# Kernel optimization log

Measured on AMD Instinct MI355X. Metric: run time of the kernel, lower is better.

## Reference

```python
import jax, jax.numpy as jnp
import numpy as np

D_MODEL = 128
NUM_HEADS = 8
DEPTH = D_MODEL // NUM_HEADS
NEG = -1e9


def _dense_params(key, d_in, d_out):
    kw, kb = jax.random.split(key)
    # Glorot-uniform like keras Dense default
    lim = np.sqrt(6.0 / (d_in + d_out))
    w = jax.random.uniform(kw, (d_in, d_out), jnp.float32, -lim, lim)
    b = jnp.zeros((d_out,), jnp.float32)
    return w, b


def setup_inputs() -> dict:
    key = jax.random.key(0)
    ks = jax.random.split(key, 16)
    B, N, M, d = 256, 128, 128, D_MODEL
    inp = {
        'x_self': jax.random.normal(ks[0], (B, N, d), jnp.float32),
        'adj_self': jax.random.randint(ks[1], (B, N, N), 0, 2, jnp.int32),
        'mask_self': jnp.ones((B, N), jnp.int32),
        'x_cross': jax.random.normal(ks[2], (B, M, d), jnp.float32),
        'mask_cross': jnp.ones((B, M), jnp.int32),
    }
    names = ['wq_s', 'wk_s', 'wv_s', 'wo_s', 'wq_c', 'wk_c', 'wv_c', 'wo_c']
    for i, nm in enumerate(names):
        w, b = _dense_params(ks[3 + i], d, d)
        inp[nm] = w
        inp['b' + nm[1:]] = b
    wg, bg = _dense_params(ks[12], 3 * d, d)
    inp['wg'] = wg
    inp['bg'] = bg
    return inp


def _split_heads(x):
    B, N, _ = x.shape
    return x.reshape(B, N, NUM_HEADS, DEPTH).transpose(0, 2, 1, 3)  # [B,H,N,depth]


def _merge_heads(x):
    B, H, N, Dp = x.shape
    return x.transpose(0, 2, 1, 3).reshape(B, N, H * Dp)


def _attention(q, k, v, mask, adj=None):
    # q,k,v: [B,H,Nq,depth]; mask: [B,Nk]; adj: [B,Nq,Nk] or None
    logits = jnp.einsum('bhqd,bhkd->bhqk', q, k) / jnp.sqrt(jnp.float32(DEPTH))
    if adj is not None:
        logits = logits + ((1.0 - adj.astype(jnp.float32)) * NEG)[:, None, :, :]
    logits = logits + ((1.0 - mask.astype(jnp.float32)) * NEG)[:, None, None, :]
    w = jax.nn.softmax(logits, axis=-1)
    return jnp.einsum('bhqk,bhkd->bhqd', w, v)


def reference(x_self, adj_self, mask_self, x_cross, mask_cross,
              wq_s, bq_s, wk_s, bk_s, wv_s, bv_s, wo_s, bo_s,
              wq_c, bq_c, wk_c, bk_c, wv_c, bv_c, wo_c, bo_c,
              wg, bg):
    # Self attention (adjacency + padding mask)
    q_s = _split_heads(x_self @ wq_s + bq_s)
    k_s = _split_heads(x_self @ wk_s + bk_s)
    v_s = _split_heads(x_self @ wv_s + bv_s)
    out_s = _merge_heads(_attention(q_s, k_s, v_s, mask_self, adj_self)) @ wo_s + bo_s
    # Cross attention (padding mask only); dropout inactive at inference
    q_c = _split_heads(x_self @ wq_c + bq_c)
    k_c = _split_heads(x_cross @ wk_c + bk_c)
    v_c = _split_heads(x_cross @ wv_c + bv_c)
    out_c = _merge_heads(_attention(q_c, k_c, v_c, mask_cross)) @ wo_c + bo_c
    # Sigmoid gate fusion
    gate = jax.nn.sigmoid(jnp.concatenate([x_self, out_s, out_c], axis=-1) @ wg + bg)
    return (1.0 - gate) * out_s + gate * out_c
```

## Files before the change

kernel.cpp:

```cpp
#include <hip/hip_runtime.h>
#include <hip/hip_bf16.h>

typedef _Float16 f16_t;
typedef __attribute__((ext_vector_type(8))) _Float16 f16x8;
typedef __attribute__((ext_vector_type(4))) float f32x4;
typedef __attribute__((ext_vector_type(16))) float f32x16;

__device__ __forceinline__ f16x8 cvt8(const float* p) {
  float4 v0 = *(const float4*)p;
  float4 v1 = *(const float4*)(p + 4);
  f16x8 a;
  a[0] = (f16_t)v0.x; a[1] = (f16_t)v0.y; a[2] = (f16_t)v0.z; a[3] = (f16_t)v0.w;
  a[4] = (f16_t)v1.x; a[5] = (f16_t)v1.y; a[6] = (f16_t)v1.z; a[7] = (f16_t)v1.w;
  return a;
}

__global__ __launch_bounds__(256) void prep_kernel(
    const float* wq_s, const float* wk_s, const float* wv_s,
    const float* wq_c, const float* wk_c, const float* wv_c,
    const float* wo_s, const float* wo_c, const float* wg,
    const float* bos, const float* boc, const float* bgin,
    f16_t* WT, float* bgp)
{
  const int b = blockIdx.x;
  const int tid = threadIdx.x;
  if (b < 11) {
    __shared__ float t[128][129];
    const float* src; f16_t* dst; int ostride;
    switch (b) {
      case 0: src = wq_s; break; case 1: src = wk_s; break;
      case 2: src = wv_s; break; case 3: src = wq_c; break;
      case 4: src = wk_c; break; case 5: src = wv_c; break;
      case 6: src = wo_s; break; case 7: src = wo_c; break;
      default: src = wg + (size_t)(b - 8) * 16384; break;
    }
    if (b < 8) { dst = WT + (size_t)b * 16384; ostride = 128; }
    else       { dst = WT + 8 * 16384 + (b - 8) * 128; ostride = 384; }
#pragma unroll
    for (int i = 0; i < 64; ++i) {
      const int idx = tid + i * 256;
      t[idx & 127][idx >> 7] = src[idx];
    }
    __syncthreads();
#pragma unroll
    for (int i = 0; i < 64; ++i) {
      const int idx = tid + i * 256;
      const int c = idx >> 7, r = idx & 127;
      dst[(size_t)c * ostride + r] = (f16_t)t[c][r];
    }
  } else if (b < 13) {
    const int matsel = b - 11;
    const float* wo = matsel ? wo_c : wo_s;
    const int joff = 128 + matsel * 128;
    f16_t* dst = WT + (size_t)(11 + matsel) * 16384;
    const int wv = tid >> 6, ln = tid & 63, l15 = ln & 15, g = ln >> 4;
    f32x4 acc[2][8];
#pragma unroll
    for (int mm = 0; mm < 2; ++mm)
#pragma unroll
      for (int nt = 0; nt < 8; ++nt) acc[mm][nt] = (f32x4){0.f, 0.f, 0.f, 0.f};
#pragma unroll
    for (int kt = 0; kt < 4; ++kt) {
      f16x8 a[2];
#pragma unroll
      for (int mm = 0; mm < 2; ++mm) {
        const int crow = wv * 32 + mm * 16 + l15;
#pragma unroll
        for (int jj = 0; jj < 8; ++jj)
          a[mm][jj] = (f16_t)wg[(size_t)(joff + kt * 32 + g * 8 + jj) * 128 + crow];
      }
#pragma unroll
      for (int nt = 0; nt < 8; ++nt) {
        f16x8 bf = cvt8(wo + (size_t)(nt * 16 + l15) * 128 + kt * 32 + g * 8);
        acc[0][nt] = __builtin_amdgcn_mfma_f32_16x16x32_f16(a[0], bf, acc[0][nt], 0, 0, 0);
        acc[1][nt] = __builtin_amdgcn_mfma_f32_16x16x32_f16(a[1], bf, acc[1][nt], 0, 0, 0);
      }
    }
#pragma unroll
    for (int mm = 0; mm < 2; ++mm)
#pragma unroll
      for (int nt = 0; nt < 8; ++nt)
#pragma unroll
        for (int r = 0; r < 4; ++r) {
          const int c = wv * 32 + mm * 16 + g * 4 + r;
          dst[(size_t)c * 128 + nt * 16 + l15] = (f16_t)acc[mm][nt][r];
        }
  } else {
    if (tid < 128) {
      float acc = bgin[tid];
      for (int j = 0; j < 128; ++j)
        acc += bos[j] * wg[(size_t)(128 + j) * 128 + tid] +
               boc[j] * wg[(size_t)(256 + j) * 128 + tid];
      bgp[tid] = acc;
    }
  }
}

template <int NW>
__device__ __forceinline__ void proj_body(
    const float* __restrict__ A, const f16_t* __restrict__ WT, int blk, int tid,
    const float* b0, f16_t* Y0, const float* b1, f16_t* Y1,
    const float* b2, f16_t* Y2, const float* b3, f16_t* Y3)
{
  const int wv = tid >> 6, ln = tid & 63, l15 = ln & 15, g = ln >> 4;
  const int rowgrp = wv & 1, colgrp = wv >> 1;
  const size_t arow = (size_t)blk * 32 + rowgrp * 16 + l15;

  f32x4 acc[NW][4];
#pragma unroll
  for (int i = 0; i < NW; ++i)
#pragma unroll
    for (int nt = 0; nt < 4; ++nt) acc[i][nt] = (f32x4){0.f, 0.f, 0.f, 0.f};

#pragma unroll
  for (int kt = 0; kt < 4; ++kt) {
    f16x8 a = cvt8(A + arow * 128 + kt * 32 + g * 8);
#pragma unroll
    for (int i = 0; i < NW; ++i)
#pragma unroll
      for (int nt = 0; nt < 4; ++nt) {
        f16x8 bfr = *(const f16x8*)(WT + (size_t)i * 16384 +
                     (size_t)(colgrp * 64 + nt * 16 + l15) * 128 + kt * 32 + g * 8);
        acc[i][nt] = __builtin_amdgcn_mfma_f32_16x16x32_f16(a, bfr, acc[i][nt], 0, 0, 0);
      }
  }

  const size_t orow0 = (size_t)blk * 32 + rowgrp * 16 + g * 4;
#pragma unroll
  for (int i = 0; i < NW; ++i) {
    const float* bp = (i == 0) ? b0 : (i == 1) ? b1 : (i == 2) ? b2 : b3;
    f16_t* Y = (i == 0) ? Y0 : (i == 1) ? Y1 : (i == 2) ? Y2 : Y3;
#pragma unroll
    for (int nt = 0; nt < 4; ++nt) {
      const int col = colgrp * 64 + nt * 16 + l15;
      const float bv = bp[col];
#pragma unroll
      for (int r = 0; r < 4; ++r)
        Y[(orow0 + r) * 128 + col] = (f16_t)(acc[i][nt][r] + bv);
    }
  }
}

__global__ __launch_bounds__(256) void projall_kernel(
    const float* __restrict__ Xs, const float* __restrict__ Xc,
    const f16_t* __restrict__ WT,
    const float* bq_s, const float* bk_s, const float* bv_s, const float* bq_c,
    const float* bk_c, const float* bv_c,
    f16_t* qs, f16_t* ks, f16_t* vs, f16_t* qc, f16_t* kc, f16_t* vc)
{
  if (blockIdx.x < 1024)
    proj_body<4>(Xs, WT, blockIdx.x, threadIdx.x,
                 bq_s, qs, bk_s, ks, bv_s, vs, bq_c, qc);
  else
    proj_body<2>(Xc, WT + 4 * 16384, blockIdx.x - 1024, threadIdx.x,
                 bk_c, kc, bv_c, vc, nullptr, nullptr, nullptr, nullptr);
}

__global__ __launch_bounds__(256) void attn4_kernel(
    const f16_t* __restrict__ Qs, const f16_t* __restrict__ Ks,
    const f16_t* __restrict__ Vs, f16_t* __restrict__ Os,
    const f16_t* __restrict__ Qc, const f16_t* __restrict__ Kc,
    const f16_t* __restrict__ Vc, f16_t* __restrict__ Oc,
    const int* __restrict__ adj, const int* __restrict__ mask_s,
    const int* __restrict__ mask_c)
{
  __shared__ __align__(16) f16_t Qh[128 * 24];
  __shared__ __align__(16) f16_t Kh[128 * 24];
  __shared__ __align__(16) f16_t Vt[16 * 136];
  __shared__ __align__(16) f16_t Pl[128 * 128];
  __shared__ float larr[128];
  __shared__ unsigned mw[4];
  __shared__ unsigned adjw[128 * 4];

  const bool self = blockIdx.x < 2048;
  const int bid = blockIdx.x & 2047;
  const int h = bid >> 8;
  const int bb = bid & 255;
  const int tid = threadIdx.x;
  const size_t base = (size_t)bb * 16384 + h * 16;
  const f16_t* Q = self ? Qs : Qc;
  const f16_t* K = self ? Ks : Kc;
  const f16_t* V = self ? Vs : Vc;
  f16_t* O = self ? Os : Oc;
  const int* mask = self ? mask_s : mask_c;

  {
    const int r = tid >> 1, hf = tid & 1;
    f16x8 qv = *(const f16x8*)(Q + base + (size_t)r * 128 + hf * 8);
    *(f16x8*)&Qh[r * 24 + hf * 8] = qv;
    f16x8 kv = *(const f16x8*)(K + base + (size_t)r * 128 + hf * 8);
    *(f16x8*)&Kh[r * 24 + hf * 8] = kv;
    f16x8 vv = *(const f16x8*)(V + base + (size_t)r * 128 + hf * 8);
#pragma unroll
    for (int j = 0; j < 8; ++j) Vt[(hf * 8 + j) * 136 + r] = vv[j];
  }
  if (tid < 128) {
    unsigned long long bm = __ballot(mask[bb * 128 + tid] != 0);
    if ((tid & 63) == 0) {
      mw[(tid >> 6) * 2 + 0] = (unsigned)bm;
      mw[(tid >> 6) * 2 + 1] = (unsigned)(bm >> 32);
    }
  }
  if (self) {
    const int r = tid >> 1, hf = tid & 1;
    const int4* ap = (const int4*)(adj + ((size_t)bb * 128 + r) * 128 + hf * 64);
    unsigned w0 = 0, w1 = 0;
#pragma unroll
    for (int i = 0; i < 8; ++i) {
      int4 a = ap[i];
      unsigned m4 = (a.x != 0 ? 1u : 0u) | (a.y != 0 ? 2u : 0u) |
                    (a.z != 0 ? 4u : 0u) | (a.w != 0 ? 8u : 0u);
      w0 |= m4 << (i * 4);
    }
#pragma unroll
    for (int i = 8; i < 16; ++i) {
      int4 a = ap[i];
      unsigned m4 = (a.x != 0 ? 1u : 0u) | (a.y != 0 ? 2u : 0u) |
                    (a.z != 0 ? 4u : 0u) | (a.w != 0 ? 8u : 0u);
      w1 |= m4 << ((i - 8) * 4);
    }
    adjw[r * 4 + hf * 2 + 0] = w0;
    adjw[r * 4 + hf * 2 + 1] = w1;
  }
  __syncthreads();

  const int ln = tid & 63;
  const int wv = tid >> 6;
  const int l31 = ln & 31;
  const int hh = ln >> 5;
  const int q = wv * 32 + l31;

  f32x16 zero16;
#pragma unroll
  for (int j = 0; j < 16; ++j) zero16[j] = 0.f;
  const f16x8 bq = *(const f16x8*)&Qh[q * 24 + hh * 8];
  f32x16 st[4];
#pragma unroll
  for (int kt = 0; kt < 4; ++kt) {
    const f16x8 ak = *(const f16x8*)&Kh[(kt * 32 + l31) * 24 + hh * 8];
    st[kt] = __builtin_amdgcn_mfma_f32_32x32x16_f16(ak, bq, zero16, 0, 0, 0);
  }

  unsigned aw[4];
#pragma unroll
  for (int kt = 0; kt < 4; ++kt)
    aw[kt] = self ? (adjw[q * 4 + kt] & mw[kt]) : mw[kt];

  const int swz = (q & 7) << 4;
  float l = 0.f;
#pragma unroll
  for (int kt = 0; kt < 4; ++kt) {
#pragma unroll
    for (int r2 = 0; r2 < 8; ++r2) {
      const int r = r2 * 2;
      const int koff = (r & 3) + 8 * (r >> 2) + 4 * hh;
      float e0 = __expf(st[kt][r]     * 0.25f - 8.f);
      float e1 = __expf(st[kt][r + 1] * 0.25f - 8.f);
      float p0 = ((aw[kt] >> koff) & 1u) ? e0 : 0.f;
      float p1 = ((aw[kt] >> (koff + 1)) & 1u) ? e1 : 0.f;
      l += p0 + p1;
      unsigned short u0 = __builtin_bit_cast(unsigned short, (f16_t)p0);
      unsigned short u1 = __builtin_bit_cast(unsigned short, (f16_t)p1);
      unsigned pk = (unsigned)u0 | ((unsigned)u1 << 16);
      const int key = kt * 32 + koff;
      *(unsigned*)((char*)Pl + q * 256 + ((key * 2) ^ swz)) = pk;
    }
  }
  l += __shfl_xor(l, 32);
  if (hh == 0) larr[q] = l;
  __syncthreads();

  const int l15 = ln & 15;
  const int g4 = ln >> 4;
  const int qa0 = wv * 32 + l15;
  const int qa1 = qa0 + 16;
  const int swz0 = (qa0 & 7) << 4;
  const int swz1 = (qa1 & 7) << 4;
  f32x4 o0 = (f32x4){0.f, 0.f, 0.f, 0.f};
  f32x4 o1 = (f32x4){0.f, 0.f, 0.f, 0.f};
#pragma unroll
  for (int kt = 0; kt < 4; ++kt) {
    const f16x8 bv = *(const f16x8*)&Vt[l15 * 136 + kt * 32 + g4 * 8];
    const f16x8 p0 = *(const f16x8*)((char*)Pl + qa0 * 256 + ((kt * 64 + g4 * 16) ^ swz0));
    const f16x8 p1 = *(const f16x8*)((char*)Pl + qa1 * 256 + ((kt * 64 + g4 * 16) ^ swz1));
    o0 = __builtin_amdgcn_mfma_f32_16x16x32_f16(p0, bv, o0, 0, 0, 0);
    o1 = __builtin_amdgcn_mfma_f32_16x16x32_f16(p1, bv, o1, 0, 0, 0);
  }
#pragma unroll
  for (int rr = 0; rr < 4; ++rr) {
    const int q0 = wv * 32 + g4 * 4 + rr;
    const int q1 = q0 + 16;
    O[base + (size_t)q0 * 128 + l15] = (f16_t)(o0[rr] / larr[q0]);
    O[base + (size_t)q1 * 128 + l15] = (f16_t)(o1[rr] / larr[q1]);
  }
}

__global__ __launch_bounds__(256) void outgate2_kernel(
    const f16_t* __restrict__ AS, const f16_t* __restrict__ AC,
    const float* __restrict__ X, const f16_t* __restrict__ WT,
    const float* __restrict__ bos, const float* __restrict__ boc,
    const float* __restrict__ bgp, float* __restrict__ OUT)
{
  const int tid = threadIdx.x;
  const int wv = tid >> 6, ln = tid & 63, l15 = ln & 15, g = ln >> 4;
  const int rowgrp = wv & 1, colgrp = wv >> 1;
  const size_t arow = (size_t)blockIdx.x * 32 + rowgrp * 16 + l15;
  const f16_t* WoS = WT + 6 * 16384;
  const f16_t* WoC = WT + 7 * 16384;
  const f16_t* WgT = WT + 8 * 16384;
  const f16_t* W2T = WT + 11 * 16384;
  const f16_t* W3T = WT + 12 * 16384;

  f32x4 accS[4], accC[4], accG[4];
#pragma unroll
  for (int nt = 0; nt < 4; ++nt) {
    accS[nt] = (f32x4){0.f, 0.f, 0.f, 0.f};
    accC[nt] = (f32x4){0.f, 0.f, 0.f, 0.f};
    accG[nt] = (f32x4){0.f, 0.f, 0.f, 0.f};
  }

#pragma unroll
  for (int kt = 0; kt < 4; ++kt) {
    const size_t ko = kt * 32 + g * 8;
    f16x8 aS = *(const f16x8*)(AS + arow * 128 + ko);
    f16x8 aC = *(const f16x8*)(AC + arow * 128 + ko);
    f16x8 aX = cvt8(X + arow * 128 + ko);
#pragma unroll
    for (int nt = 0; nt < 4; ++nt) {
      const size_t col = colgrp * 64 + nt * 16 + l15;
      f16x8 bS = *(const f16x8*)(WoS + col * 128 + ko);
      f16x8 bC = *(const f16x8*)(WoC + col * 128 + ko);
      f16x8 b2 = *(const f16x8*)(W2T + col * 128 + ko);
      f16x8 b3 = *(const f16x8*)(W3T + col * 128 + ko);
      f16x8 bX = *(const f16x8*)(WgT + col * 384 + ko);
      accS[nt] = __builtin_amdgcn_mfma_f32_16x16x32_f16(aS, bS, accS[nt], 0, 0, 0);
      accC[nt] = __builtin_amdgcn_mfma_f32_16x16x32_f16(aC, bC, accC[nt], 0, 0, 0);
      accG[nt] = __builtin_amdgcn_mfma_f32_16x16x32_f16(aX, bX, accG[nt], 0, 0, 0);
      accG[nt] = __builtin_amdgcn_mfma_f32_16x16x32_f16(aS, b2, accG[nt], 0, 0, 0);
      accG[nt] = __builtin_amdgcn_mfma_f32_16x16x32_f16(aC, b3, accG[nt], 0, 0, 0);
    }
  }

  const size_t orow0 = (size_t)blockIdx.x * 32 + rowgrp * 16 + g * 4;
#pragma unroll
  for (int nt = 0; nt < 4; ++nt) {
    const int col = colgrp * 64 + nt * 16 + l15;
    const float bS = bos[col], bC = boc[col], bG = bgp[col];
#pragma unroll
    for (int r = 0; r < 4; ++r) {
      const float os = accS[nt][r] + bS;
      const float oc = accC[nt][r] + bC;
      const float gv = 1.f / (1.f + __expf(-(accG[nt][r] + bG)));
      OUT[(orow0 + r) * 128 + col] = (1.f - gv) * os + gv * oc;
    }
  }
}

extern "C" void kernel_launch(void* const* d_in, const int* in_sizes, int n_in,
                              void* d_out, int out_size, void* d_ws, size_t ws_size,
                              hipStream_t stream)
{
  const float* x_self  = (const float*)d_in[0];
  const int*   adj     = (const int*)d_in[1];
  const int*   mask_s  = (const int*)d_in[2];
  const float* x_cross = (const float*)d_in[3];
  const int*   mask_c  = (const int*)d_in[4];
  const float* wq_s = (const float*)d_in[5];
  const float* bq_s = (const float*)d_in[6];
  const float* wk_s = (const float*)d_in[7];
  const float* bk_s = (const float*)d_in[8];
  const float* wv_s = (const float*)d_in[9];
  const float* bv_s = (const float*)d_in[10];
  const float* wo_s = (const float*)d_in[11];
  const float* bo_s = (const float*)d_in[12];
  const float* wq_c = (const float*)d_in[13];
  const float* bq_c = (const float*)d_in[14];
  const float* wk_c = (const float*)d_in[15];
  const float* bk_c = (const float*)d_in[16];
  const float* wv_c = (const float*)d_in[17];
  const float* bv_c = (const float*)d_in[18];
  const float* wo_c = (const float*)d_in[19];
  const float* bo_c = (const float*)d_in[20];
  const float* wg   = (const float*)d_in[21];
  const float* bg   = (const float*)d_in[22];
  float* out = (float*)d_out;

  const size_t SZ = (size_t)256 * 128 * 128;
  f16_t* w16 = (f16_t*)d_ws;
  f16_t* qs  = w16 + 0 * SZ;
  f16_t* ks  = w16 + 1 * SZ;
  f16_t* vs  = w16 + 2 * SZ;
  f16_t* qc  = w16 + 3 * SZ;
  f16_t* kc  = w16 + 4 * SZ;
  f16_t* vc  = w16 + 5 * SZ;
  f16_t* as_ = w16 + 6 * SZ;
  f16_t* ac_ = w16 + 7 * SZ;
  f16_t* WT  = w16 + 8 * SZ;
  float* bgp = (float*)(WT + 13 * 16384);

  prep_kernel<<<14, 256, 0, stream>>>(wq_s, wk_s, wv_s, wq_c, wk_c, wv_c,
                                      wo_s, wo_c, wg, bo_s, bo_c, bg, WT, bgp);
  projall_kernel<<<2048, 256, 0, stream>>>(x_self, x_cross, WT,
                                           bq_s, bk_s, bv_s, bq_c, bk_c, bv_c,
                                           qs, ks, vs, qc, kc, vc);
  attn4_kernel<<<4096, 256, 0, stream>>>(qs, ks, vs, as_, qc, kc, vc, ac_,
                                         adj, mask_s, mask_c);
  outgate2_kernel<<<1024, 256, 0, stream>>>(as_, ac_, x_self, WT,
                                            bo_s, bo_c, bgp, out);
}
```

Baseline: 159.2 us.

## Fuse projections, both attentions and output gate into one per-batch kernel

Replaces the projection, attention and output-gate kernels with a single kernel: one 512-thread block per batch element. Q/K/V and the attention outputs now live in swizzled LDS buffers instead of f16 global intermediates, and each wave walks all 8 heads for its 16 query rows. This is meant to remove the global write and re-read of eight intermediate tensors and two kernel launches. The cost is about 144KB of LDS per block, so likely one block per CU and only 256 blocks, plus a long serial chain of GEMM and attention phases separated by barriers. Weights are still read from global/L2 inside every block.

```diff
diff --git a/kernel.cpp b/kernel.cpp
--- a/kernel.cpp
+++ b/kernel.cpp
@@ -4,7 +4,6 @@
 typedef _Float16 f16_t;
 typedef __attribute__((ext_vector_type(8))) _Float16 f16x8;
 typedef __attribute__((ext_vector_type(4))) float f32x4;
-typedef __attribute__((ext_vector_type(16))) float f32x16;
 
 __device__ __forceinline__ f16x8 cvt8(const float* p) {
   float4 v0 = *(const float4*)p;
@@ -96,262 +95,250 @@
   }
 }
 
-template <int NW>
-__device__ __forceinline__ void proj_body(
-    const float* __restrict__ A, const f16_t* __restrict__ WT, int blk, int tid,
-    const float* b0, f16_t* Y0, const float* b1, f16_t* Y1,
-    const float* b2, f16_t* Y2, const float* b3, f16_t* Y3)
-{
+template <bool TRANSP>
+__device__ __forceinline__ void gemm_w(
+    const f16x8 afr[4], const f16_t* __restrict__ W, const float* __restrict__ bias,
+    char* Ob, int l15, int g, int wv)
+{
+  f32x4 acc[8];
+#pragma unroll
+  for (int nt = 0; nt < 8; ++nt) acc[nt] = (f32x4){0.f, 0.f, 0.f, 0.f};
+#pragma unroll
+  for (int nt = 0; nt < 8; ++nt)
+#pragma unroll
+    for (int kt = 0; kt < 4; ++kt) {
+      f16x8 b = *(const f16x8*)(W + (size_t)(nt * 16 + l15) * 128 + kt * 32 + g * 8);
+      acc[nt] = __builtin_amdgcn_mfma_f32_16x16x32_f16(afr[kt], b, acc[nt], 0, 0, 0);
+    }
+#pragma unroll
+  for (int nt = 0; nt < 8; ++nt) {
+    const int col = nt * 16 + l15;
+    const float bv = bias[col];
+#pragma unroll
+    for (int r = 0; r < 4; ++r) {
+      const int row = wv * 16 + g * 4 + r;
+      const f16_t v = (f16_t)(acc[nt][r] + bv);
+      if (TRANSP)
+        *(f16_t*)(Ob + col * 256 + ((row * 2) ^ ((col & 7) << 4))) = v;
+      else
+        *(f16_t*)(Ob + row * 256 + ((col * 2) ^ ((row & 7) << 4))) = v;
+    }
+  }
+}
+
+__device__ __forceinline__ void attn_wave(
+    char* Qb, const char* Kb, const char* Vtb, const unsigned aw[4],
+    char* Pw, int l15, int g, int wv)
+{
+  const int q = wv * 16 + l15;
+  const int qsw = (q & 7) << 4;
+  const int psw = (l15 & 7) << 4;
+  const f32x4 zero = (f32x4){0.f, 0.f, 0.f, 0.f};
+
+#pragma unroll
+  for (int h = 0; h < 8; ++h) {
+    f16x8 bq = {0, 0, 0, 0, 0, 0, 0, 0};
+    if (g < 2) bq = *(const f16x8*)(Qb + q * 256 + ((h * 32 + g * 16) ^ qsw));
+    f32x4 st[8];
+#pragma unroll
+    for (int kt = 0; kt < 8; ++kt) {
+      const int krow = kt * 16 + l15;
+      f16x8 ak = {0, 0, 0, 0, 0, 0, 0, 0};
+      if (g < 2)
+        ak = *(const f16x8*)(Kb + krow * 256 + ((h * 32 + g * 16) ^ ((krow & 7) << 4)));
+      st[kt] = __builtin_amdgcn_mfma_f32_16x16x32_f16(ak, bq, zero, 0, 0, 0);
+    }
+    float psum = 0.f;
+#pragma unroll
+    for (int kt = 0; kt < 8; ++kt)
+#pragma unroll
+      for (int r = 0; r < 4; ++r) {
+        const int k = kt * 16 + g * 4 + r;
+        const float e = __expf(st[kt][r] * 0.25f - 8.f);
+        const float p = ((aw[kt >> 1] >> (k & 31)) & 1u) ? e : 0.f;
+        psum += p;
+        st[kt][r] = p;
+      }
+    psum += __shfl_xor(psum, 16);
+    psum += __shfl_xor(psum, 32);
+    const float inv = 1.f / psum;
+
+    f32x4 o = zero;
+#pragma unroll
+    for (int half = 0; half < 2; ++half) {
+#pragma unroll
+      for (int kt2 = 0; kt2 < 4; ++kt2) {
+        const int kt = half * 4 + kt2;
+        union { f16_t hh[4]; unsigned long long u; } pk;
+#pragma unroll
+        for (int r = 0; r < 4; ++r) pk.hh[r] = (f16_t)(st[kt][r] * inv);
+        *(unsigned long long*)(Pw + l15 * 128 + ((kt2 * 32 + g * 8) ^ psw)) = pk.u;
+      }
+#pragma unroll
+      for (int kt32 = 0; kt32 < 2; ++kt32) {
+        f16x8 pa = *(const f16x8*)(Pw + l15 * 128 + ((kt32 * 64 + g * 16) ^ psw));
+        const int d = h * 16 + l15;
+        f16x8 vb = *(const f16x8*)(Vtb + d * 256 +
+                     (((half * 64 + kt32 * 32 + g * 8) * 2) ^ ((d & 7) << 4)));
+        o = __builtin_amdgcn_mfma_f32_16x16x32_f16(pa, vb, o, 0, 0, 0);
+      }
+    }
+#pragma unroll
+    for (int r = 0; r < 4; ++r) {
+      const int qo = wv * 16 + g * 4 + r;
+      *(f16_t*)(Qb + qo * 256 + (((h * 16 + l15) * 2) ^ ((qo & 7) << 4))) = (f16_t)o[r];
+    }
+  }
+}
+
+__global__ __launch_bounds__(512, 2) void fused_kernel(
+    const float* __restrict__ Xs_g, const float* __restrict__ Xc_g,
+    const int* __restrict__ adj, const int* __restrict__ mask_s,
+    const int* __restrict__ mask_c, const f16_t* __restrict__ WT,
+    const float* __restrict__ bq_s, const float* __restrict__ bk_s,
+    const float* __restrict__ bv_s, const float* __restrict__ bq_c,
+    const float* __restrict__ bk_c, const float* __restrict__ bv_c,
+    const float* __restrict__ bos, const float* __restrict__ boc,
+    const float* __restrict__ bgp, float* __restrict__ OUT)
+{
+  __shared__ __align__(16) char B0[32768];
+  __shared__ __align__(16) char B1[32768];
+  __shared__ __align__(16) char B2[32768];
+  __shared__ __align__(16) char B3[32768];
+  __shared__ __align__(16) char PR[16384];
+  __shared__ unsigned mw_s[4], mwc_s[4];
+
+  const int bb = blockIdx.x;
+  const int tid = threadIdx.x;
   const int wv = tid >> 6, ln = tid & 63, l15 = ln & 15, g = ln >> 4;
-  const int rowgrp = wv & 1, colgrp = wv >> 1;
-  const size_t arow = (size_t)blk * 32 + rowgrp * 16 + l15;
-
-  f32x4 acc[NW][4];
-#pragma unroll
-  for (int i = 0; i < NW; ++i)
-#pragma unroll
-    for (int nt = 0; nt < 4; ++nt) acc[i][nt] = (f32x4){0.f, 0.f, 0.f, 0.f};
-
-#pragma unroll
-  for (int kt = 0; kt < 4; ++kt) {
-    f16x8 a = cvt8(A + arow * 128 + kt * 32 + g * 8);
-#pragma unroll
-    for (int i = 0; i < NW; ++i)
-#pragma unroll
-      for (int nt = 0; nt < 4; ++nt) {
-        f16x8 bfr = *(const f16x8*)(WT + (size_t)i * 16384 +
-                     (size_t)(colgrp * 64 + nt * 16 + l15) * 128 + kt * 32 + g * 8);
-        acc[i][nt] = __builtin_amdgcn_mfma_f32_16x16x32_f16(a, bfr, acc[i][nt], 0, 0, 0);
-      }
-  }
-
-  const size_t orow0 = (size_t)blk * 32 + rowgrp * 16 + g * 4;
-#pragma unroll
-  for (int i = 0; i < NW; ++i) {
-    const float* bp = (i == 0) ? b0 : (i == 1) ? b1 : (i == 2) ? b2 : b3;
-    f16_t* Y = (i == 0) ? Y0 : (i == 1) ? Y1 : (i == 2) ? Y2 : Y3;
-#pragma unroll
-    for (int nt = 0; nt < 4; ++nt) {
-      const int col = colgrp * 64 + nt * 16 + l15;
-      const float bv = bp[col];
-#pragma unroll
-      for (int r = 0; r < 4; ++r)
-        Y[(orow0 + r) * 128 + col] = (f16_t)(acc[i][nt][r] + bv);
-    }
-  }
-}
-
-__global__ __launch_bounds__(256) void projall_kernel(
-    const float* __restrict__ Xs, const float* __restrict__ Xc,
-    const f16_t* __restrict__ WT,
-    const float* bq_s, const float* bk_s, const float* bv_s, const float* bq_c,
-    const float* bk_c, const float* bv_c,
-    f16_t* qs, f16_t* ks, f16_t* vs, f16_t* qc, f16_t* kc, f16_t* vc)
-{
-  if (blockIdx.x < 1024)
-    proj_body<4>(Xs, WT, blockIdx.x, threadIdx.x,
-                 bq_s, qs, bk_s, ks, bv_s, vs, bq_c, qc);
-  else
-    proj_body<2>(Xc, WT + 4 * 16384, blockIdx.x - 1024, threadIdx.x,
-                 bk_c, kc, bv_c, vc, nullptr, nullptr, nullptr, nullptr);
-}
-
-__global__ __launch_bounds__(256) void attn4_kernel(
-    const f16_t* __restrict__ Qs, const f16_t* __restrict__ Ks,
-    const f16_t* __restrict__ Vs, f16_t* __restrict__ Os,
-    const f16_t* __restrict__ Qc, const f16_t* __restrict__ Kc,
-    const f16_t* __restrict__ Vc, f16_t* __restrict__ Oc,
-    const int* __restrict__ adj, const int* __restrict__ mask_s,
-    const int* __restrict__ mask_c)
-{
-  __shared__ __align__(16) f16_t Qh[128 * 24];
-  __shared__ __align__(16) f16_t Kh[128 * 24];
-  __shared__ __align__(16) f16_t Vt[16 * 136];
-  __shared__ __align__(16) f16_t Pl[128 * 128];
-  __shared__ float larr[128];
-  __shared__ unsigned mw[4];
-  __shared__ unsigned adjw[128 * 4];
-
-  const bool self = blockIdx.x < 2048;
-  const int bid = blockIdx.x & 2047;
-  const int h = bid >> 8;
-  const int bb = bid & 255;
-  const int tid = threadIdx.x;
-  const size_t base = (size_t)bb * 16384 + h * 16;
-  const f16_t* Q = self ? Qs : Qc;
-  const f16_t* K = self ? Ks : Kc;
-  const f16_t* V = self ? Vs : Vc;
-  f16_t* O = self ? Os : Oc;
-  const int* mask = self ? mask_s : mask_c;
-
-  {
-    const int r = tid >> 1, hf = tid & 1;
-    f16x8 qv = *(const f16x8*)(Q + base + (size_t)r * 128 + hf * 8);
-    *(f16x8*)&Qh[r * 24 + hf * 8] = qv;
-    f16x8 kv = *(const f16x8*)(K + base + (size_t)r * 128 + hf * 8);
-    *(f16x8*)&Kh[r * 24 + hf * 8] = kv;
-    f16x8 vv = *(const f16x8*)(V + base + (size_t)r * 128 + hf * 8);
-#pragma unroll
-    for (int j = 0; j < 8; ++j) Vt[(hf * 8 + j) * 136 + r] = vv[j];
-  }
-  if (tid < 128) {
-    unsigned long long bm = __ballot(mask[bb * 128 + tid] != 0);
-    if ((tid & 63) == 0) {
-      mw[(tid >> 6) * 2 + 0] = (unsigned)bm;
-      mw[(tid >> 6) * 2 + 1] = (unsigned)(bm >> 32);
-    }
-  }
-  if (self) {
-    const int r = tid >> 1, hf = tid & 1;
-    const int4* ap = (const int4*)(adj + ((size_t)bb * 128 + r) * 128 + hf * 64);
-    unsigned w0 = 0, w1 = 0;
+
+  {
+    const int r = tid >> 2, c0 = (tid & 3) * 32;
+    const float* src = Xs_g + (size_t)bb * 16384 + r * 128 + c0;
+    const int sw = (r & 7) << 4;
+#pragma unroll
+    for (int i = 0; i < 4; ++i) {
+      f16x8 v = cvt8(src + i * 8);
+      *(f16x8*)(B3 + r * 256 + ((c0 * 2 + i * 16) ^ sw)) = v;
+    }
+    const int4* ap = (const int4*)(adj + (size_t)bb * 16384 + r * 128 + (tid & 3) * 32);
+    unsigned bits = 0;
 #pragma unroll
     for (int i = 0; i < 8; ++i) {
       int4 a = ap[i];
-      unsigned m4 = (a.x != 0 ? 1u : 0u) | (a.y != 0 ? 2u : 0u) |
-                    (a.z != 0 ? 4u : 0u) | (a.w != 0 ? 8u : 0u);
-      w0 |= m4 << (i * 4);
-    }
-#pragma unroll
-    for (int i = 8; i < 16; ++i) {
-      int4 a = ap[i];
-      unsigned m4 = (a.x != 0 ? 1u : 0u) | (a.y != 0 ? 2u : 0u) |
-                    (a.z != 0 ? 4u : 0u) | (a.w != 0 ? 8u : 0u);
-      w1 |= m4 << ((i - 8) * 4);
-    }
-    adjw[r * 4 + hf * 2 + 0] = w0;
-    adjw[r * 4 + hf * 2 + 1] = w1;
-  }
-  __syncthreads();
-
-  const int ln = tid & 63;
-  const int wv = tid >> 6;
-  const int l31 = ln & 31;
-  const int hh = ln >> 5;
-  const int q = wv * 32 + l31;
-
-  f32x16 zero16;
-#pragma unroll
-  for (int j = 0; j < 16; ++j) zero16[j] = 0.f;
-  const f16x8 bq = *(const f16x8*)&Qh[q * 24 + hh * 8];
-  f32x16 st[4];
-#pragma unroll
-  for (int kt = 0; kt < 4; ++kt) {
-    const f16x8 ak = *(const f16x8*)&Kh[(kt * 32 + l31) * 24 + hh * 8];
-    st[kt] = __builtin_amdgcn_mfma_f32_32x32x16_f16(ak, bq, zero16, 0, 0, 0);
-  }
-
-  unsigned aw[4];
-#pragma unroll
-  for (int kt = 0; kt < 4; ++kt)
-    aw[kt] = self ? (adjw[q * 4 + kt] & mw[kt]) : mw[kt];
-
-  const int swz = (q & 7) << 4;
-  float l = 0.f;
-#pragma unroll
-  for (int kt = 0; kt < 4; ++kt) {
-#pragma unroll
-    for (int r2 = 0; r2 < 8; ++r2) {
-      const int r = r2 * 2;
-      const int koff = (r & 3) + 8 * (r >> 2) + 4 * hh;
-      float e0 = __expf(st[kt][r]     * 0.25f - 8.f);
-      float e1 = __expf(st[kt][r + 1] * 0.25f - 8.f);
-      float p0 = ((aw[kt] >> koff) & 1u) ? e0 : 0.f;
-      float p1 = ((aw[kt] >> (koff + 1)) & 1u) ? e1 : 0.f;
-      l += p0 + p1;
-      unsigned short u0 = __builtin_bit_cast(unsigned short, (f16_t)p0);
-      unsigned short u1 = __builtin_bit_cast(unsigned short, (f16_t)p1);
-      unsigned pk = (unsigned)u0 | ((unsigned)u1 << 16);
-      const int key = kt * 32 + koff;
-      *(unsigned*)((char*)Pl + q * 256 + ((key * 2) ^ swz)) = pk;
-    }
-  }
-  l += __shfl_xor(l, 32);
-  if (hh == 0) larr[q] = l;
-  __syncthreads();
-
-  const int l15 = ln & 15;
-  const int g4 = ln >> 4;
-  const int qa0 = wv * 32 + l15;
-  const int qa1 = qa0 + 16;
-  const int swz0 = (qa0 & 7) << 4;
-  const int swz1 = (qa1 & 7) << 4;
-  f32x4 o0 = (f32x4){0.f, 0.f, 0.f, 0.f};
-  f32x4 o1 = (f32x4){0.f, 0.f, 0.f, 0.f};
-#pragma unroll
-  for (int kt = 0; kt < 4; ++kt) {
-    const f16x8 bv = *(const f16x8*)&Vt[l15 * 136 + kt * 32 + g4 * 8];
-    const f16x8 p0 = *(const f16x8*)((char*)Pl + qa0 * 256 + ((kt * 64 + g4 * 16) ^ swz0));
-    const f16x8 p1 = *(const f16x8*)((char*)Pl + qa1 * 256 + ((kt * 64 + g4 * 16) ^ swz1));
-    o0 = __builtin_amdgcn_mfma_f32_16x16x32_f16(p0, bv, o0, 0, 0, 0);
-    o1 = __builtin_amdgcn_mfma_f32_16x16x32_f16(p1, bv, o1, 0, 0, 0);
-  }
-#pragma unroll
-  for (int rr = 0; rr < 4; ++rr) {
-    const int q0 = wv * 32 + g4 * 4 + rr;
-    const int q1 = q0 + 16;
-    O[base + (size_t)q0 * 128 + l15] = (f16_t)(o0[rr] / larr[q0]);
-    O[base + (size_t)q1 * 128 + l15] = (f16_t)(o1[rr] / larr[q1]);
-  }
-}
-
-__global__ __launch_bounds__(256) void outgate2_kernel(
-    const f16_t* __restrict__ AS, const f16_t* __restrict__ AC,
-    const float* __restrict__ X, const f16_t* __restrict__ WT,
-    const float* __restrict__ bos, const float* __restrict__ boc,
-    const float* __restrict__ bgp, float* __restrict__ OUT)
-{
-  const int tid = threadIdx.x;
-  const int wv = tid >> 6, ln = tid & 63, l15 = ln & 15, g = ln >> 4;
-  const int rowgrp = wv & 1, colgrp = wv >> 1;
-  const size_t arow = (size_t)blockIdx.x * 32 + rowgrp * 16 + l15;
-  const f16_t* WoS = WT + 6 * 16384;
-  const f16_t* WoC = WT + 7 * 16384;
-  const f16_t* WgT = WT + 8 * 16384;
-  const f16_t* W2T = WT + 11 * 16384;
-  const f16_t* W3T = WT + 12 * 16384;
-
-  f32x4 accS[4], accC[4], accG[4];
-#pragma unroll
-  for (int nt = 0; nt < 4; ++nt) {
-    accS[nt] = (f32x4){0.f, 0.f, 0.f, 0.f};
-    accC[nt] = (f32x4){0.f, 0.f, 0.f, 0.f};
-    accG[nt] = (f32x4){0.f, 0.f, 0.f, 0.f};
-  }
-
-#pragma unroll
-  for (int kt = 0; kt < 4; ++kt) {
-    const size_t ko = kt * 32 + g * 8;
-    f16x8 aS = *(const f16x8*)(AS + arow * 128 + ko);
-    f16x8 aC = *(const f16x8*)(AC + arow * 128 + ko);
-    f16x8 aX = cvt8(X + arow * 128 + ko);
-#pragma unroll
-    for (int nt = 0; nt < 4; ++nt) {
-      const size_t col = colgrp * 64 + nt * 16 + l15;
-      f16x8 bS = *(const f16x8*)(WoS + col * 128 + ko);
-      f16x8 bC = *(const f16x8*)(WoC + col * 128 + ko);
-      f16x8 b2 = *(const f16x8*)(W2T + col * 128 + ko);
-      f16x8 b3 = *(const f16x8*)(W3T + col * 128 + ko);
-      f16x8 bX = *(const f16x8*)(WgT + col * 384 + ko);
-      accS[nt] = __builtin_amdgcn_mfma_f32_16x16x32_f16(aS, bS, accS[nt], 0, 0, 0);
-      accC[nt] = __builtin_amdgcn_mfma_f32_16x16x32_f16(aC, bC, accC[nt], 0, 0, 0);
-      accG[nt] = __builtin_amdgcn_mfma_f32_16x16x32_f16(aX, bX, accG[nt], 0, 0, 0);
-      accG[nt] = __builtin_amdgcn_mfma_f32_16x16x32_f16(aS, b2, accG[nt], 0, 0, 0);
-      accG[nt] = __builtin_amdgcn_mfma_f32_16x16x32_f16(aC, b3, accG[nt], 0, 0, 0);
-    }
-  }
-
-  const size_t orow0 = (size_t)blockIdx.x * 32 + rowgrp * 16 + g * 4;
-#pragma unroll
-  for (int nt = 0; nt < 4; ++nt) {
-    const int col = colgrp * 64 + nt * 16 + l15;
-    const float bS = bos[col], bC = boc[col], bG = bgp[col];
-#pragma unroll
-    for (int r = 0; r < 4; ++r) {
-      const float os = accS[nt][r] + bS;
-      const float oc = accC[nt][r] + bC;
-      const float gv = 1.f / (1.f + __expf(-(accG[nt][r] + bG)));
-      OUT[(orow0 + r) * 128 + col] = (1.f - gv) * os + gv * oc;
+      bits |= ((a.x != 0 ? 1u : 0u) | (a.y != 0 ? 2u : 0u) |
+               (a.z != 0 ? 4u : 0u) | (a.w != 0 ? 8u : 0u)) << (i * 4);
+    }
+    *(unsigned*)(PR + r * 16 + (tid & 3) * 4) = bits;
+  }
+  if (tid < 128) {
+    unsigned long long bm = __ballot(mask_s[bb * 128 + tid] != 0);
+    if ((tid & 63) == 0) {
+      mw_s[(tid >> 6) * 2 + 0] = (unsigned)bm;
+      mw_s[(tid >> 6) * 2 + 1] = (unsigned)(bm >> 32);
+    }
+  } else if (tid < 256) {
+    const int t = tid - 128;
+    unsigned long long bm = __ballot(mask_c[bb * 128 + t] != 0);
+    if ((t & 63) == 0) {
+      mwc_s[(t >> 6) * 2 + 0] = (unsigned)bm;
+      mwc_s[(t >> 6) * 2 + 1] = (unsigned)(bm >> 32);
+    }
+  }
+  __syncthreads();
+
+  {
+    const int arow = wv * 16 + l15;
+    const int asw = (arow & 7) << 4;
+    f16x8 afr[4];
+#pragma unroll
+    for (int kt = 0; kt < 4; ++kt)
+      afr[kt] = *(const f16x8*)(B3 + arow * 256 + ((kt * 64 + g * 16) ^ asw));
+    gemm_w<false>(afr, WT + 0 * 16384, bq_s, B0, l15, g, wv);
+    gemm_w<false>(afr, WT + 1 * 16384, bk_s, B1, l15, g, wv);
+    gemm_w<true >(afr, WT + 2 * 16384, bv_s, B2, l15, g, wv);
+    gemm_w<false>(afr, WT + 3 * 16384, bq_c, B3, l15, g, wv);
+  }
+  __syncthreads();
+
+  {
+    const int q_own = wv * 16 + l15;
+    const uint4 a4 = *(const uint4*)(PR + q_own * 16);
+    unsigned aw[4] = {a4.x & mw_s[0], a4.y & mw_s[1], a4.z & mw_s[2], a4.w & mw_s[3]};
+    __syncthreads();
+    attn_wave(B0, B1, B2, aw, PR + wv * 2048, l15, g, wv);
+  }
+  __syncthreads();
+
+  {
+    const int arow = wv * 16 + l15;
+    f16x8 afr[4];
+#pragma unroll
+    for (int kt = 0; kt < 4; ++kt)
+      afr[kt] = cvt8(Xc_g + (size_t)bb * 16384 + arow * 128 + kt * 32 + g * 8);
+    gemm_w<false>(afr, WT + 4 * 16384, bk_c, B1, l15, g, wv);
+    gemm_w<true >(afr, WT + 5 * 16384, bv_c, B2, l15, g, wv);
+  }
+  __syncthreads();
+
+  {
+    unsigned awc[4] = {mwc_s[0], mwc_s[1], mwc_s[2], mwc_s[3]};
+    attn_wave(B3, B1, B2, awc, PR + wv * 2048, l15, g, wv);
+  }
+  __syncthreads();
+
+  {
+    const int arow = wv * 16 + l15;
+    const int asw = (arow & 7) << 4;
+    f16x8 aS[4], aC[4], aX[4];
+#pragma unroll
+    for (int kt = 0; kt < 4; ++kt) {
+      aS[kt] = *(const f16x8*)(B0 + arow * 256 + ((kt * 64 + g * 16) ^ asw));
+      aC[kt] = *(const f16x8*)(B3 + arow * 256 + ((kt * 64 + g * 16) ^ asw));
+      aX[kt] = cvt8(Xs_g + (size_t)bb * 16384 + arow * 128 + kt * 32 + g * 8);
+    }
+    const f16_t* WoS = WT + 6 * 16384;
+    const f16_t* WoC = WT + 7 * 16384;
+    const f16_t* Wg1 = WT + 8 * 16384;
+    const f16_t* W2p = WT + 11 * 16384;
+    const f16_t* W3p = WT + 12 * 16384;
+    f32x4 accS[8], accC[8], accG[8];
+#pragma unroll
+    for (int nt = 0; nt < 8; ++nt) {
+      accS[nt] = (f32x4){0.f, 0.f, 0.f, 0.f};
+      accC[nt] = (f32x4){0.f, 0.f, 0.f, 0.f};
+      accG[nt] = (f32x4){0.f, 0.f, 0.f, 0.f};
+    }
+#pragma unroll
+    for (int nt = 0; nt < 8; ++nt) {
+      const size_t col = nt * 16 + l15;
+#pragma unroll
+      for (int kt = 0; kt < 4; ++kt) {
+        const size_t ko = kt * 32 + g * 8;
+        f16x8 bS = *(const f16x8*)(WoS + col * 128 + ko);
+        f16x8 bC = *(const f16x8*)(WoC + col * 128 + ko);
+        f16x8 bG = *(const f16x8*)(Wg1 + col * 384 + ko);
+        f16x8 b2 = *(const f16x8*)(W2p + col * 128 + ko);
+        f16x8 b3 = *(const f16x8*)(W3p + col * 128 + ko);
+        accS[nt] = __builtin_amdgcn_mfma_f32_16x16x32_f16(aS[kt], bS, accS[nt], 0, 0, 0);
+        accC[nt] = __builtin_amdgcn_mfma_f32_16x16x32_f16(aC[kt], bC, accC[nt], 0, 0, 0);
+        accG[nt] = __builtin_amdgcn_mfma_f32_16x16x32_f16(aX[kt], bG, accG[nt], 0, 0, 0);
+        accG[nt] = __builtin_amdgcn_mfma_f32_16x16x32_f16(aS[kt], b2, accG[nt], 0, 0, 0);
+        accG[nt] = __builtin_amdgcn_mfma_f32_16x16x32_f16(aC[kt], b3, accG[nt], 0, 0, 0);
+      }
+    }
+#pragma unroll
+    for (int nt = 0; nt < 8; ++nt) {
+      const int col = nt * 16 + l15;
+      const float bS = bos[col], bC = boc[col], bG = bgp[col];
+#pragma unroll
+      for (int r = 0; r < 4; ++r) {
+        const int row = wv * 16 + g * 4 + r;
+        const float os = accS[nt][r] + bS;
+        const float oc = accC[nt][r] + bC;
+        const float gv = 1.f / (1.f + __expf(-(accG[nt][r] + bG)));
+        OUT[(size_t)bb * 16384 + row * 128 + col] = (1.f - gv) * os + gv * oc;
+      }
     }
   }
 }
@@ -385,26 +372,12 @@
   const float* bg   = (const float*)d_in[22];
   float* out = (float*)d_out;
 
-  const size_t SZ = (size_t)256 * 128 * 128;
-  f16_t* w16 = (f16_t*)d_ws;
-  f16_t* qs  = w16 + 0 * SZ;
-  f16_t* ks  = w16 + 1 * SZ;
-  f16_t* vs  = w16 + 2 * SZ;
-  f16_t* qc  = w16 + 3 * SZ;
-  f16_t* kc  = w16 + 4 * SZ;
-  f16_t* vc  = w16 + 5 * SZ;
-  f16_t* as_ = w16 + 6 * SZ;
-  f16_t* ac_ = w16 + 7 * SZ;
-  f16_t* WT  = w16 + 8 * SZ;
+  f16_t* WT  = (f16_t*)d_ws;
   float* bgp = (float*)(WT + 13 * 16384);
 
   prep_kernel<<<14, 256, 0, stream>>>(wq_s, wk_s, wv_s, wq_c, wk_c, wv_c,
                                       wo_s, wo_c, wg, bo_s, bo_c, bg, WT, bgp);
-  projall_kernel<<<2048, 256, 0, stream>>>(x_self, x_cross, WT,
-                                           bq_s, bk_s, bv_s, bq_c, bk_c, bv_c,
-                                           qs, ks, vs, qc, kc, vc);
-  attn4_kernel<<<4096, 256, 0, stream>>>(qs, ks, vs, as_, qc, kc, vc, ac_,
-                                         adj, mask_s, mask_c);
-  outgate2_kernel<<<1024, 256, 0, stream>>>(as_, ac_, x_self, WT,
-                                            bo_s, bo_c, bgp, out);
-}
+  fused_kernel<<<256, 512, 0, stream>>>(x_self, x_cross, adj, mask_s, mask_c, WT,
+                                        bq_s, bk_s, bv_s, bq_c, bk_c, bv_c,
+                                        bo_s, bo_c, bgp, out);
+}
```

Result: faster. 132.8 us (-16.6%).
